# Optimization experiments

Measured on AMD Instinct MI355X. Metric: run time of the kernel, lower is better.

The kernel has to match this reference:

```python
import jax, jax.numpy as jnp
import numpy as np

B, S, DM, H = 4, 4096, 1024, 16
HD = DM // H

def setup_inputs() -> dict:
    key = jax.random.key(0)
    ks = jax.random.split(key, 9)
    sc = 1.0 / np.sqrt(DM)
    return {
        "x": jax.random.normal(ks[0], (B, S, DM), dtype=jnp.float32),
        "Wq": jax.random.normal(ks[1], (DM, DM), dtype=jnp.float32) * sc,
        "bq": jnp.zeros((DM,), dtype=jnp.float32),
        "Wk": jax.random.normal(ks[2], (DM, DM), dtype=jnp.float32) * sc,
        "bk": jnp.zeros((DM,), dtype=jnp.float32),
        "Wv": jax.random.normal(ks[3], (DM, DM), dtype=jnp.float32) * sc,
        "bv": jnp.zeros((DM,), dtype=jnp.float32),
        "Wo": jax.random.normal(ks[4], (DM, DM), dtype=jnp.float32) * sc,
        "bo": jnp.zeros((DM,), dtype=jnp.float32),
    }

def _heads(t):
    # [B,S,DM] -> [B,H,S,HD]
    return t.reshape(B, S, H, HD).transpose(0, 2, 1, 3)

def reference(x, Wq, bq, Wk, bk, Wv, bv, Wo, bo):
    q = _heads(x @ Wq.T + bq)
    k = _heads(x @ Wk.T + bk)
    v = _heads(x @ Wv.T + bv)
    q = jax.nn.elu(q) + 1.0  # positive feature map
    k = jax.nn.elu(k) + 1.0
    # kv aggregation: [B,H,HD,HD]
    kv = jnp.einsum('bhsd,bhse->bhde', k, v)
    qkv = jnp.einsum('bhsd,bhde->bhse', q, kv)  # [B,H,S,HD]
    k_sum = k.sum(axis=2)  # [B,H,HD]
    normalizer = jnp.einsum('bhsd,bhd->bhs', q, k_sum) + 1e-6
    out = qkv / normalizer[..., None]
    out = out.transpose(0, 2, 1, 3).reshape(B, S, DM)
    return out @ Wo.T + bo  # dropout is identity in eval
```

## Files before the change

kernel.cpp:

```cpp
#include <hip/hip_runtime.h>
#include <math.h>

#define NROWS  16384
#define DMODEL 1024
#define NHEAD  16
#define HDIM   64
#define SEQ    4096
#define NBATCH 4
#define NBH    64
#define SCHUNK 16
#define M1     1048576u

typedef __attribute__((ext_vector_type(8)))  short bf16x8;
typedef __attribute__((ext_vector_type(4)))  float f32x4;
typedef __attribute__((ext_vector_type(16))) float f32x16;

#define VMCNT(N) asm volatile("s_waitcnt vmcnt(" #N ")" ::: "memory")
#define BAR() do { asm volatile("" ::: "memory"); __builtin_amdgcn_s_barrier(); \
                   asm volatile("" ::: "memory"); } while (0)

__device__ __forceinline__ unsigned short f2bf(float f) {
    unsigned u = __float_as_uint(f);
    u += 0x7FFFu + ((u >> 16) & 1u);
    return (unsigned short)(u >> 16);
}
__device__ __forceinline__ float bf2f(unsigned short h) {
    return __uint_as_float((unsigned)h << 16);
}

__device__ __forceinline__ void gload16(const void* g, void* l) {
    __builtin_amdgcn_global_load_lds(
        (const __attribute__((address_space(1))) unsigned int*)g,
        (__attribute__((address_space(3))) unsigned int*)l, 16, 0, 0);
}

__global__ __launch_bounds__(256)
void split_pair(const float* __restrict__ a, unsigned short* __restrict__ hi,
                unsigned short* __restrict__ lo, int n4)
{
    int i = blockIdx.x * 256 + threadIdx.x;
    const int stride = gridDim.x * 256;
    for (; i < n4; i += stride) {
        const float4 v = ((const float4*)a)[i];
        ushort4 H, L;
        H.x = f2bf(v.x); L.x = f2bf(v.x - bf2f(H.x));
        H.y = f2bf(v.y); L.y = f2bf(v.y - bf2f(H.y));
        H.z = f2bf(v.z); L.z = f2bf(v.z - bf2f(H.z));
        H.w = f2bf(v.w); L.w = f2bf(v.w - bf2f(H.w));
        ((ushort4*)hi)[i] = H;
        ((ushort4*)lo)[i] = L;
    }
}

__global__ __launch_bounds__(256)
void split_w4(const float* __restrict__ a0, const float* __restrict__ a1,
              const float* __restrict__ a2, const float* __restrict__ a3,
              unsigned short* __restrict__ hib, unsigned short* __restrict__ lob)
{
    const int y = blockIdx.y;
    const float* src = (y == 0) ? a0 : (y == 1) ? a1 : (y == 2) ? a2 : a3;
    const int i = blockIdx.x * 256 + threadIdx.x;
    const float4 v = ((const float4*)src)[i];
    ushort4 H, L;
    H.x = f2bf(v.x); L.x = f2bf(v.x - bf2f(H.x));
    H.y = f2bf(v.y); L.y = f2bf(v.y - bf2f(H.y));
    H.z = f2bf(v.z); L.z = f2bf(v.z - bf2f(H.z));
    H.w = f2bf(v.w); L.w = f2bf(v.w - bf2f(H.w));
    const size_t o = (size_t)y * M1 + (size_t)i * 4;
    *(ushort4*)&hib[o] = H;
    *(ushort4*)&lob[o] = L;
}

template<int MODE>
__global__ __launch_bounds__(512)
void gemm32(const unsigned short* __restrict__ Ah, const unsigned short* __restrict__ Al,
            const unsigned short* __restrict__ Wh, const unsigned short* __restrict__ Wl,
            const float* __restrict__ bias0, const float* __restrict__ bias1,
            float* __restrict__ C0, float* __restrict__ C1, int nbs)
{
    __shared__ unsigned short lds[32768];
    const int t    = threadIdx.x;
    const int lane = t & 63;
    const int wv   = t >> 6;
    const int wr   = wv >> 2;
    const int wcn  = wv & 3;

    const int bid = blockIdx.x;
    const int swz = (bid & 7) * ((int)gridDim.x >> 3) + (bid >> 3);
    const int mb  = swz >> nbs;
    const int nb  = swz & ((1 << nbs) - 1);
    const int am0 = mb * 256;
    const int bn0 = nb * 256;

    const int l31  = lane & 31;
    const int hi5  = lane >> 5;
    const unsigned fro = (unsigned)lane * 8u;

    f32x16 acc[4][2];
#pragma unroll
    for (int i = 0; i < 4; ++i)
#pragma unroll
        for (int j = 0; j < 2; ++j)
#pragma unroll
            for (int e = 0; e < 16; ++e) acc[i][j][e] = 0.f;

    auto stageA = [&](int kt) {
        const unsigned bb = ((unsigned)kt & 1u) * 16384u;
        const size_t g = (size_t)(am0 + wv * 32 + l31) * DMODEL + kt * 16 + hi5 * 8;
        gload16(Ah + g, (unsigned short*)&lds[bb + (unsigned)wv * 512u]);
        gload16(Al + g, (unsigned short*)&lds[bb + 4096u + (unsigned)wv * 512u]);
    };
    auto stageW = [&](int kt) {
        const unsigned bb = ((unsigned)kt & 1u) * 16384u;
        const size_t g = (size_t)(bn0 + wv * 32 + l31) * DMODEL + kt * 16 + hi5 * 8;
        gload16(Wh + g, (unsigned short*)&lds[bb + 8192u  + (unsigned)wv * 512u]);
        gload16(Wl + g, (unsigned short*)&lds[bb + 12288u + (unsigned)wv * 512u]);
    };

    stageA(0); stageW(0); stageW(1);

#pragma unroll 2
    for (int kt = 0; kt < 64; ++kt) {
        if (kt < 63) { VMCNT(2); } else { VMCNT(0); }
        BAR();
        const unsigned bb = ((unsigned)kt & 1u) * 16384u;

        bf16x8 bh[2], bl[2];
#pragma unroll
        for (int ni = 0; ni < 2; ++ni) {
            const unsigned ch = (unsigned)(wcn * 2 + ni) * 512u;
            bh[ni] = *(const bf16x8*)&lds[bb + 8192u  + ch + fro];
            bl[ni] = *(const bf16x8*)&lds[bb + 12288u + ch + fro];
        }
        bf16x8 ah[2], al[2];
#pragma unroll
        for (int i2 = 0; i2 < 2; ++i2) {
            const unsigned ch = (unsigned)(wr * 4 + i2) * 512u;
            ah[i2] = *(const bf16x8*)&lds[bb + ch + fro];
            al[i2] = *(const bf16x8*)&lds[bb + 4096u + ch + fro];
        }
        if (kt + 1 < 64) stageA(kt + 1);
        __builtin_amdgcn_s_barrier();
        __builtin_amdgcn_s_setprio(1);
#pragma unroll
        for (int i2 = 0; i2 < 2; ++i2)
#pragma unroll
            for (int ni = 0; ni < 2; ++ni) {
                acc[i2][ni] = __builtin_amdgcn_mfma_f32_32x32x16_bf16(ah[i2], bh[ni], acc[i2][ni], 0, 0, 0);
                acc[i2][ni] = __builtin_amdgcn_mfma_f32_32x32x16_bf16(ah[i2], bl[ni], acc[i2][ni], 0, 0, 0);
                acc[i2][ni] = __builtin_amdgcn_mfma_f32_32x32x16_bf16(al[i2], bh[ni], acc[i2][ni], 0, 0, 0);
            }
        __builtin_amdgcn_s_setprio(0);

#pragma unroll
        for (int i2 = 0; i2 < 2; ++i2) {
            const unsigned ch = (unsigned)(wr * 4 + 2 + i2) * 512u;
            ah[i2] = *(const bf16x8*)&lds[bb + ch + fro];
            al[i2] = *(const bf16x8*)&lds[bb + 4096u + ch + fro];
        }
        __builtin_amdgcn_s_barrier();
        if (kt + 2 < 64) stageW(kt + 2);
        __builtin_amdgcn_s_setprio(1);
#pragma unroll
        for (int i2 = 0; i2 < 2; ++i2)
#pragma unroll
            for (int ni = 0; ni < 2; ++ni) {
                acc[2 + i2][ni] = __builtin_amdgcn_mfma_f32_32x32x16_bf16(ah[i2], bh[ni], acc[2 + i2][ni], 0, 0, 0);
                acc[2 + i2][ni] = __builtin_amdgcn_mfma_f32_32x32x16_bf16(ah[i2], bl[ni], acc[2 + i2][ni], 0, 0, 0);
                acc[2 + i2][ni] = __builtin_amdgcn_mfma_f32_32x32x16_bf16(al[i2], bh[ni], acc[2 + i2][ni], 0, 0, 0);
            }
        __builtin_amdgcn_s_setprio(0);
    }

    bool elu = (MODE == 1);
    float* Cm = C0;
    const float* bm = bias0;
    int colb = bn0;
    if (MODE == 2) {
        if (nb < 4) { elu = true; }
        else        { Cm = C1; bm = bias1; colb = (nb - 4) * 256; }
    }
    const int crow00 = am0 + wr * 128 + 4 * hi5;
#pragma unroll
    for (int ni = 0; ni < 2; ++ni) {
        const int col = colb + wcn * 64 + ni * 32 + l31;
        const float bv = bm[col];
#pragma unroll
        for (int mi = 0; mi < 4; ++mi) {
#pragma unroll
            for (int r = 0; r < 16; ++r) {
                const int row = crow00 + mi * 32 + (r & 3) + 8 * (r >> 2);
                float v = acc[mi][ni][r] + bv;
                if (elu) v = (v > 0.f) ? (v + 1.f) : __expf(v);
                Cm[(size_t)row * DMODEL + col] = v;
            }
        }
    }
}

__global__ __launch_bounds__(512)
void kv_partial(const float* __restrict__ k, const float* __restrict__ v,
                float* __restrict__ kvp, float* __restrict__ ksp)
{
    __shared__ float Ks[32][64];
    __shared__ float Vs[32][64];
    const int t  = threadIdx.x;
    const int bh = blockIdx.x;
    const int b  = bh >> 4;
    const int h  = bh & 15;
    const int sc = blockIdx.y;
    const int d  = t & 63;
    const int e0 = (t >> 6) * 8;

    float acc[8];
#pragma unroll
    for (int j = 0; j < 8; ++j) acc[j] = 0.f;
    float ks = 0.f;

    const size_t rowbase = (size_t)b * SEQ;
    const int sbeg = sc * (SEQ / SCHUNK);
    const int send = sbeg + (SEQ / SCHUNK);
    const int lrow = t >> 4;
    const int lc4  = (t & 15) * 4;

    for (int s0 = sbeg; s0 < send; s0 += 32) {
        const size_t g = (rowbase + s0 + lrow) * DMODEL + h * HDIM + lc4;
        *(float4*)&Ks[lrow][lc4] = *(const float4*)&k[g];
        *(float4*)&Vs[lrow][lc4] = *(const float4*)&v[g];
        __syncthreads();
#pragma unroll 8
        for (int sp = 0; sp < 32; ++sp) {
            const float kd = Ks[sp][d];
            if (t < 64) ks += Ks[sp][t];
            const float4 v0 = *(const float4*)&Vs[sp][e0 + 0];
            const float4 v1 = *(const float4*)&Vs[sp][e0 + 4];
            acc[0] = fmaf(kd, v0.x, acc[0]);  acc[1] = fmaf(kd, v0.y, acc[1]);
            acc[2] = fmaf(kd, v0.z, acc[2]);  acc[3] = fmaf(kd, v0.w, acc[3]);
            acc[4] = fmaf(kd, v1.x, acc[4]);  acc[5] = fmaf(kd, v1.y, acc[5]);
            acc[6] = fmaf(kd, v1.z, acc[6]);  acc[7] = fmaf(kd, v1.w, acc[7]);
        }
        __syncthreads();
    }

    const size_t base = ((size_t)sc * NBH + bh) * HDIM;
    float4 o0; o0.x = acc[0]; o0.y = acc[1]; o0.z = acc[2]; o0.w = acc[3];
    float4 o1; o1.x = acc[4]; o1.y = acc[5]; o1.z = acc[6]; o1.w = acc[7];
    *(float4*)&kvp[(base + d) * HDIM + e0 + 0] = o0;
    *(float4*)&kvp[(base + d) * HDIM + e0 + 4] = o1;
    if (t < 64) ksp[base + t] = ks;
}

__global__ __launch_bounds__(256)
void kv_reduce(const float* __restrict__ kvp, const float* __restrict__ ksp,
               float* __restrict__ kv, float* __restrict__ ksum)
{
    const int i = blockIdx.x * 256 + threadIdx.x;
    const int NKV = NBH * HDIM * HDIM;
    if (i < NKV) {
        float s = 0.f;
#pragma unroll
        for (int c = 0; c < SCHUNK; ++c) s += kvp[(size_t)c * NKV + i];
        kv[i] = s;
    }
    if (i < NBH * HDIM) {
        float s = 0.f;
#pragma unroll
        for (int c = 0; c < SCHUNK; ++c) s += ksp[(size_t)c * NBH * HDIM + i];
        ksum[i] = s;
    }
}

__global__ __launch_bounds__(256)
void qkv_norm(const float* __restrict__ q, const float* __restrict__ kv,
              const float* __restrict__ ksum,
              unsigned short* __restrict__ ah, unsigned short* __restrict__ al)
{
    __shared__ float Qs[64][68];
    __shared__ float KVs[64][64];
    __shared__ float kss[64];
    const int t  = threadIdx.x;
    const int s0 = blockIdx.x * 64;
    const int b  = blockIdx.y;
    const int h  = blockIdx.z;
    const int bh = b * NHEAD + h;

#pragma unroll
    for (int i = 0; i < 4; ++i) {
        const int idx = i * 256 + t;
        const int row = idx >> 4;
        const int c4  = (idx & 15) * 4;
        const float4 vq = *(const float4*)&q[((size_t)b * SEQ + s0 + row) * DMODEL + h * HDIM + c4];
        *(float4*)&Qs[row][c4] = vq;
        *(float4*)&((float*)KVs)[idx * 4] = *(const float4*)&kv[(size_t)bh * HDIM * HDIM + idx * 4];
    }
    if (t < 64) kss[t] = ksum[(size_t)bh * HDIM + t];
    __syncthreads();

    const int r  = t >> 2;
    const int e0 = (t & 3) * 16;
    float out[16];
#pragma unroll
    for (int j = 0; j < 16; ++j) out[j] = 0.f;
    float nrm = 0.f;

#pragma unroll 8
    for (int d = 0; d < 64; ++d) {
        const float qd = Qs[r][d];
        nrm = fmaf(qd, kss[d], nrm);
        const float4 k0 = *(const float4*)&KVs[d][e0 + 0];
        const float4 k1 = *(const float4*)&KVs[d][e0 + 4];
        const float4 k2 = *(const float4*)&KVs[d][e0 + 8];
        const float4 k3 = *(const float4*)&KVs[d][e0 + 12];
        out[0]  = fmaf(qd, k0.x, out[0]);  out[1]  = fmaf(qd, k0.y, out[1]);
        out[2]  = fmaf(qd, k0.z, out[2]);  out[3]  = fmaf(qd, k0.w, out[3]);
        out[4]  = fmaf(qd, k1.x, out[4]);  out[5]  = fmaf(qd, k1.y, out[5]);
        out[6]  = fmaf(qd, k1.z, out[6]);  out[7]  = fmaf(qd, k1.w, out[7]);
        out[8]  = fmaf(qd, k2.x, out[8]);  out[9]  = fmaf(qd, k2.y, out[9]);
        out[10] = fmaf(qd, k2.z, out[10]); out[11] = fmaf(qd, k2.w, out[11]);
        out[12] = fmaf(qd, k3.x, out[12]); out[13] = fmaf(qd, k3.y, out[13]);
        out[14] = fmaf(qd, k3.z, out[14]); out[15] = fmaf(qd, k3.w, out[15]);
    }

    const float inv = 1.f / (nrm + 1e-6f);
    const size_t gbase = ((size_t)b * SEQ + s0 + r) * DMODEL + h * HDIM + e0;
#pragma unroll
    for (int g4 = 0; g4 < 4; ++g4) {
        ushort4 H, L;
        const float v0 = out[g4*4+0] * inv;
        const float v1 = out[g4*4+1] * inv;
        const float v2 = out[g4*4+2] * inv;
        const float v3 = out[g4*4+3] * inv;
        H.x = f2bf(v0); L.x = f2bf(v0 - bf2f(H.x));
        H.y = f2bf(v1); L.y = f2bf(v1 - bf2f(H.y));
        H.z = f2bf(v2); L.z = f2bf(v2 - bf2f(H.z));
        H.w = f2bf(v3); L.w = f2bf(v3 - bf2f(H.w));
        *(ushort4*)&ah[gbase + g4 * 4] = H;
        *(ushort4*)&al[gbase + g4 * 4] = L;
    }
}

extern "C" void kernel_launch(void* const* d_in, const int* in_sizes, int n_in,
                              void* d_out, int out_size, void* d_ws, size_t ws_size,
                              hipStream_t stream)
{
    const float* x  = (const float*)d_in[0];
    const float* Wq = (const float*)d_in[1];
    const float* bq = (const float*)d_in[2];
    const float* Wk = (const float*)d_in[3];
    const float* bk = (const float*)d_in[4];
    const float* Wv = (const float*)d_in[5];
    const float* bv = (const float*)d_in[6];
    const float* Wo = (const float*)d_in[7];
    const float* bo = (const float*)d_in[8];

    unsigned short* xh  = (unsigned short*)d_ws;
    unsigned short* xl  = xh + (size_t)NROWS * DMODEL;
    unsigned short* whi = xl + (size_t)NROWS * DMODEL;
    unsigned short* wlo = whi + 4u * M1;
    float* buf0 = (float*)(wlo + 4u * M1);
    float* kv   = buf0 + (size_t)NROWS * DMODEL;
    float* ksum = kv + NBH * HDIM * HDIM;
    float* kvp  = ksum + NBH * HDIM;
    float* ksp  = kvp + (size_t)SCHUNK * NBH * HDIM * HDIM;
    float* vbuf = (float*)d_out;

    const int n4x = NROWS * DMODEL / 4;

    split_w4<<<dim3(1024, 4), 256, 0, stream>>>(Wk, Wv, Wq, Wo, whi, wlo);
    split_pair<<<4096, 256, 0, stream>>>(x, xh, xl, n4x);
    gemm32<2><<<512, 512, 0, stream>>>(xh, xl, whi, wlo, bk, bv, buf0, vbuf, 3);
    kv_partial<<<dim3(NBH, SCHUNK), 512, 0, stream>>>(buf0, vbuf, kvp, ksp);
    kv_reduce<<<1024, 256, 0, stream>>>(kvp, ksp, kv, ksum);
    gemm32<1><<<256, 512, 0, stream>>>(xh, xl, whi + 2u * M1, wlo + 2u * M1,
                                       bq, nullptr, buf0, nullptr, 2);
    qkv_norm<<<dim3(SEQ / 64, NBATCH, NHEAD), 256, 0, stream>>>(buf0, kv, ksum, xh, xl);
    gemm32<0><<<256, 512, 0, stream>>>(xh, xl, whi + 3u * M1, wlo + 3u * M1,
                                       bo, nullptr, (float*)d_out, nullptr, 2);
}
```

Baseline: 536.7 us.

## Replace shared-tile GEMM with per-wave private 64x64 tiles without block barriers

The 256x256 block-tiled split-bf16 GEMM, where eight waves share double-buffered LDS tiles and sync with s_barrier, is replaced by a kernel in which each wave owns a private 64x64 output tile. Each wave stages its own A and W hi/lo planes into its own LDS region with an XOR swizzle, so workgroup barriers disappear and waits are only vmcnt/lgkmcnt. The aim is to remove barrier stalls and LDS bank conflicts. The cost is no sharing of A or W tiles between waves, so global/L2 traffic rises, and there is only a single LDS buffer with a full vmcnt(0) wait each k-step, which limits overlap of loads and MFMA.

```diff
diff --git a/kernel.cpp b/kernel.cpp
--- a/kernel.cpp
+++ b/kernel.cpp
@@ -16,8 +16,7 @@
 typedef __attribute__((ext_vector_type(16))) float f32x16;
 
 #define VMCNT(N) asm volatile("s_waitcnt vmcnt(" #N ")" ::: "memory")
-#define BAR() do { asm volatile("" ::: "memory"); __builtin_amdgcn_s_barrier(); \
-                   asm volatile("" ::: "memory"); } while (0)
+#define LGKM0()  asm volatile("s_waitcnt lgkmcnt(0)" ::: "memory")
 
 __device__ __forceinline__ unsigned short f2bf(float f) {
     unsigned u = __float_as_uint(f);
@@ -73,123 +72,107 @@
 
 template<int MODE>
 __global__ __launch_bounds__(512)
-void gemm32(const unsigned short* __restrict__ Ah, const unsigned short* __restrict__ Al,
-            const unsigned short* __restrict__ Wh, const unsigned short* __restrict__ Wl,
-            const float* __restrict__ bias0, const float* __restrict__ bias1,
-            float* __restrict__ C0, float* __restrict__ C1, int nbs)
-{
-    __shared__ unsigned short lds[32768];
-    const int t    = threadIdx.x;
-    const int lane = t & 63;
-    const int wv   = t >> 6;
-    const int wr   = wv >> 2;
-    const int wcn  = wv & 3;
-
-    const int bid = blockIdx.x;
-    const int swz = (bid & 7) * ((int)gridDim.x >> 3) + (bid >> 3);
-    const int mb  = swz >> nbs;
-    const int nb  = swz & ((1 << nbs) - 1);
-    const int am0 = mb * 256;
-    const int bn0 = nb * 256;
-
-    const int l31  = lane & 31;
-    const int hi5  = lane >> 5;
-    const unsigned fro = (unsigned)lane * 8u;
-
-    f32x16 acc[4][2];
-#pragma unroll
-    for (int i = 0; i < 4; ++i)
+void gemm_pw(const unsigned short* __restrict__ Ah, const unsigned short* __restrict__ Al,
+             const unsigned short* __restrict__ Wh, const unsigned short* __restrict__ Wl,
+             const float* __restrict__ bias0, const float* __restrict__ bias1,
+             float* __restrict__ C0, float* __restrict__ C1)
+{
+    __shared__ unsigned short lds[65536];
+    const int t   = threadIdx.x;
+    const int l   = t & 63;
+    const int wv  = t >> 6;
+    const int l31 = l & 31;
+    const int hi5 = l >> 5;
+
+    int jm, jn;
+    {
+        const int bid = blockIdx.x;
+        if (MODE == 2) { const int swz = (bid & 7) * 128 + (bid >> 3);
+                         jm = swz >> 2; jn = (swz & 3) * 8 + wv; }
+        else           { const int swz = (bid & 7) * 64 + (bid >> 3);
+                         jm = swz >> 1; jn = (swz & 1) * 8 + wv; }
+    }
+    const int arow0 = jm * 64;
+    const int brow0 = jn * 64;
+    const unsigned wbu = (unsigned)wv * 8192u;
+
+    auto stage_plane = [&](const unsigned short* gs, int rb, unsigned po, int k0u) {
+#pragma unroll
+        for (int g = 0; g < 4; ++g) {
+            const int row  = g * 16 + (l >> 2);
+            const int srcu = ((l & 3) ^ (row & 3)) << 3;
+            gload16(gs + (size_t)(rb + row) * 1024 + k0u + srcu,
+                    (unsigned short*)&lds[wbu + po + (unsigned)(g * 512 + l * 8)]);
+        }
+    };
+    auto stage_tile = [&](int kt) {
+        const int k0u = kt * 32;
+        stage_plane(Ah, arow0, 0u,    k0u);
+        stage_plane(Al, arow0, 2048u, k0u);
+        stage_plane(Wh, brow0, 4096u, k0u);
+        stage_plane(Wl, brow0, 6144u, k0u);
+    };
+
+    f32x16 acc[2][2];
+#pragma unroll
+    for (int i = 0; i < 2; ++i)
 #pragma unroll
         for (int j = 0; j < 2; ++j)
 #pragma unroll
             for (int e = 0; e < 16; ++e) acc[i][j][e] = 0.f;
 
-    auto stageA = [&](int kt) {
-        const unsigned bb = ((unsigned)kt & 1u) * 16384u;
-        const size_t g = (size_t)(am0 + wv * 32 + l31) * DMODEL + kt * 16 + hi5 * 8;
-        gload16(Ah + g, (unsigned short*)&lds[bb + (unsigned)wv * 512u]);
-        gload16(Al + g, (unsigned short*)&lds[bb + 4096u + (unsigned)wv * 512u]);
-    };
-    auto stageW = [&](int kt) {
-        const unsigned bb = ((unsigned)kt & 1u) * 16384u;
-        const size_t g = (size_t)(bn0 + wv * 32 + l31) * DMODEL + kt * 16 + hi5 * 8;
-        gload16(Wh + g, (unsigned short*)&lds[bb + 8192u  + (unsigned)wv * 512u]);
-        gload16(Wl + g, (unsigned short*)&lds[bb + 12288u + (unsigned)wv * 512u]);
-    };
-
-    stageA(0); stageW(0); stageW(1);
-
-#pragma unroll 2
-    for (int kt = 0; kt < 64; ++kt) {
-        if (kt < 63) { VMCNT(2); } else { VMCNT(0); }
-        BAR();
-        const unsigned bb = ((unsigned)kt & 1u) * 16384u;
-
-        bf16x8 bh[2], bl[2];
-#pragma unroll
-        for (int ni = 0; ni < 2; ++ni) {
-            const unsigned ch = (unsigned)(wcn * 2 + ni) * 512u;
-            bh[ni] = *(const bf16x8*)&lds[bb + 8192u  + ch + fro];
-            bl[ni] = *(const bf16x8*)&lds[bb + 12288u + ch + fro];
-        }
-        bf16x8 ah[2], al[2];
-#pragma unroll
-        for (int i2 = 0; i2 < 2; ++i2) {
-            const unsigned ch = (unsigned)(wr * 4 + i2) * 512u;
-            ah[i2] = *(const bf16x8*)&lds[bb + ch + fro];
-            al[i2] = *(const bf16x8*)&lds[bb + 4096u + ch + fro];
-        }
-        if (kt + 1 < 64) stageA(kt + 1);
-        __builtin_amdgcn_s_barrier();
+    stage_tile(0);
+
+    for (int kt = 0; kt < 32; ++kt) {
+        VMCNT(0);
+        __builtin_amdgcn_sched_barrier(0);
+        bf16x8 af[2][2][2], bf[2][2][2];
+#pragma unroll
+        for (int kh = 0; kh < 2; ++kh)
+#pragma unroll
+            for (int blk = 0; blk < 2; ++blk) {
+                const unsigned row = (unsigned)(blk * 32 + l31);
+                const unsigned ko  = (unsigned)((kh * 16 + hi5 * 8) ^ ((l31 & 3) << 3));
+                af[kh][blk][0] = *(const bf16x8*)&lds[wbu + 0u    + row * 32u + ko];
+                af[kh][blk][1] = *(const bf16x8*)&lds[wbu + 2048u + row * 32u + ko];
+                bf[kh][blk][0] = *(const bf16x8*)&lds[wbu + 4096u + row * 32u + ko];
+                bf[kh][blk][1] = *(const bf16x8*)&lds[wbu + 6144u + row * 32u + ko];
+            }
+        LGKM0();
+        __builtin_amdgcn_sched_barrier(0);
+        if (kt < 31) stage_tile(kt + 1);
         __builtin_amdgcn_s_setprio(1);
 #pragma unroll
-        for (int i2 = 0; i2 < 2; ++i2)
-#pragma unroll
-            for (int ni = 0; ni < 2; ++ni) {
-                acc[i2][ni] = __builtin_amdgcn_mfma_f32_32x32x16_bf16(ah[i2], bh[ni], acc[i2][ni], 0, 0, 0);
-                acc[i2][ni] = __builtin_amdgcn_mfma_f32_32x32x16_bf16(ah[i2], bl[ni], acc[i2][ni], 0, 0, 0);
-                acc[i2][ni] = __builtin_amdgcn_mfma_f32_32x32x16_bf16(al[i2], bh[ni], acc[i2][ni], 0, 0, 0);
-            }
-        __builtin_amdgcn_s_setprio(0);
-
-#pragma unroll
-        for (int i2 = 0; i2 < 2; ++i2) {
-            const unsigned ch = (unsigned)(wr * 4 + 2 + i2) * 512u;
-            ah[i2] = *(const bf16x8*)&lds[bb + ch + fro];
-            al[i2] = *(const bf16x8*)&lds[bb + 4096u + ch + fro];
-        }
-        __builtin_amdgcn_s_barrier();
-        if (kt + 2 < 64) stageW(kt + 2);
-        __builtin_amdgcn_s_setprio(1);
-#pragma unroll
-        for (int i2 = 0; i2 < 2; ++i2)
-#pragma unroll
-            for (int ni = 0; ni < 2; ++ni) {
-                acc[2 + i2][ni] = __builtin_amdgcn_mfma_f32_32x32x16_bf16(ah[i2], bh[ni], acc[2 + i2][ni], 0, 0, 0);
-                acc[2 + i2][ni] = __builtin_amdgcn_mfma_f32_32x32x16_bf16(ah[i2], bl[ni], acc[2 + i2][ni], 0, 0, 0);
-                acc[2 + i2][ni] = __builtin_amdgcn_mfma_f32_32x32x16_bf16(al[i2], bh[ni], acc[2 + i2][ni], 0, 0, 0);
-            }
+        for (int kh = 0; kh < 2; ++kh)
+#pragma unroll
+            for (int mi = 0; mi < 2; ++mi)
+#pragma unroll
+                for (int ni = 0; ni < 2; ++ni) {
+                    acc[mi][ni] = __builtin_amdgcn_mfma_f32_32x32x16_bf16(af[kh][mi][0], bf[kh][ni][0], acc[mi][ni], 0, 0, 0);
+                    acc[mi][ni] = __builtin_amdgcn_mfma_f32_32x32x16_bf16(af[kh][mi][0], bf[kh][ni][1], acc[mi][ni], 0, 0, 0);
+                    acc[mi][ni] = __builtin_amdgcn_mfma_f32_32x32x16_bf16(af[kh][mi][1], bf[kh][ni][0], acc[mi][ni], 0, 0, 0);
+                }
         __builtin_amdgcn_s_setprio(0);
     }
 
     bool elu = (MODE == 1);
     float* Cm = C0;
     const float* bm = bias0;
-    int colb = bn0;
+    int colb = brow0;
     if (MODE == 2) {
-        if (nb < 4) { elu = true; }
-        else        { Cm = C1; bm = bias1; colb = (nb - 4) * 256; }
-    }
-    const int crow00 = am0 + wr * 128 + 4 * hi5;
+        if (jn < 16) { elu = true; }
+        else         { Cm = C1; bm = bias1; colb = brow0 - 1024; }
+    }
+    const int r0 = arow0 + 4 * hi5;
 #pragma unroll
     for (int ni = 0; ni < 2; ++ni) {
-        const int col = colb + wcn * 64 + ni * 32 + l31;
+        const int col = colb + ni * 32 + l31;
         const float bv = bm[col];
 #pragma unroll
-        for (int mi = 0; mi < 4; ++mi) {
+        for (int mi = 0; mi < 2; ++mi) {
 #pragma unroll
             for (int r = 0; r < 16; ++r) {
-                const int row = crow00 + mi * 32 + (r & 3) + 8 * (r >> 2);
+                const int row = r0 + mi * 32 + (r & 3) + 8 * (r >> 2);
                 float v = acc[mi][ni][r] + bv;
                 if (elu) v = (v > 0.f) ? (v + 1.f) : __expf(v);
                 Cm[(size_t)row * DMODEL + col] = v;
@@ -368,12 +351,12 @@
 
     split_w4<<<dim3(1024, 4), 256, 0, stream>>>(Wk, Wv, Wq, Wo, whi, wlo);
     split_pair<<<4096, 256, 0, stream>>>(x, xh, xl, n4x);
-    gemm32<2><<<512, 512, 0, stream>>>(xh, xl, whi, wlo, bk, bv, buf0, vbuf, 3);
+    gemm_pw<2><<<1024, 512, 0, stream>>>(xh, xl, whi, wlo, bk, bv, buf0, vbuf);
     kv_partial<<<dim3(NBH, SCHUNK), 512, 0, stream>>>(buf0, vbuf, kvp, ksp);
     kv_reduce<<<1024, 256, 0, stream>>>(kvp, ksp, kv, ksum);
-    gemm32<1><<<256, 512, 0, stream>>>(xh, xl, whi + 2u * M1, wlo + 2u * M1,
-                                       bq, nullptr, buf0, nullptr, 2);
+    gemm_pw<1><<<512, 512, 0, stream>>>(xh, xl, whi + 2u * M1, wlo + 2u * M1,
+                                        bq, nullptr, buf0, nullptr);
     qkv_norm<<<dim3(SEQ / 64, NBATCH, NHEAD), 256, 0, stream>>>(buf0, kv, ksum, xh, xl);
-    gemm32<0><<<256, 512, 0, stream>>>(xh, xl, whi + 3u * M1, wlo + 3u * M1,
-                                       bo, nullptr, (float*)d_out, nullptr, 2);
-}
+    gemm_pw<0><<<512, 512, 0, stream>>>(xh, xl, whi + 3u * M1, wlo + 3u * M1,
+                                        bo, nullptr, (float*)d_out, nullptr);
+}
```

Result: slower. 780.1 us (+45.3%).
